# Kernel tuning notes

Measured on AMD Instinct MI355X. Metric: run time of the kernel, lower is better.

Reference implementation:

```python
import jax, jax.numpy as jnp
import numpy as np

REG_COEF = 25.0


def _reflect(points, planes):
    # points: [B,P,3], planes: [B,4] -> reflected points [B,P,3]
    normals = planes[:, 0:3] / jnp.linalg.norm(planes[:, 0:3], axis=1, keepdims=True)
    offsets = planes[:, 3]
    # signed distance of each point to the plane: [B,P]
    dist = jnp.einsum('bd,bpd->bp', normals, points) + offsets[:, None]
    return points - 2.0 * dist[..., None] * normals[:, None, :]


def _chamfer(x, y):
    # x,y: [B,P,3]; pytorch3d chamfer_distance default:
    # mean over points, mean over batch, sum of both directions (squared dists)
    x2 = jnp.sum(x * x, axis=-1)  # [B,P]
    y2 = jnp.sum(y * y, axis=-1)  # [B,P]
    # pairwise squared distances [B,P,P]
    d = x2[:, :, None] + y2[:, None, :] - 2.0 * jnp.einsum('bpd,bqd->bpq', x, y)
    d = jnp.maximum(d, 0.0)
    cham_x = jnp.mean(jnp.min(d, axis=2))  # x -> nearest in y
    cham_y = jnp.mean(jnp.min(d, axis=1))  # y -> nearest in x
    return cham_x + cham_y


def _reg_loss(planes):
    # planes: [B,H,4]
    normals = planes[:, :, :3]
    normals = normals / jnp.linalg.norm(normals, axis=2, keepdims=True)
    H = normals.shape[1]
    a = jnp.einsum('bhd,bgd->bhg', normals, normals) - jnp.eye(H, dtype=normals.dtype)
    # Frobenius norm per batch -> [B]
    return jnp.sqrt(jnp.sum(a * a, axis=(1, 2)))


def setup_inputs() -> dict:
    key = jax.random.key(0)
    k1, k2 = jax.random.split(key)
    B, H, P = 8, 3, 4096
    return {
        'predicted_planes': jax.random.normal(k1, (B, H, 4), dtype=jnp.float32),
        'sample_points': jax.random.normal(k2, (B, P, 3), dtype=jnp.float32),
        'voxel_grids': jnp.zeros((B, 32, 32, 32), dtype=jnp.float32),
        'cp_grids': jnp.zeros((B, 32, 32, 32), dtype=jnp.float32),
    }


def reference(predicted_planes, sample_points, voxel_grids, cp_grids):
    n_heads = predicted_planes.shape[1]
    reg = jnp.sum(_reg_loss(predicted_planes))
    refl = jnp.asarray(0.0, dtype=sample_points.dtype)
    for h in range(n_heads):  # small fixed head count (3)
        reflected = _reflect(sample_points, predicted_planes[:, h, :])
        refl = refl + _chamfer(sample_points, reflected)
    return refl + REG_COEF * reg
```

## Files before the change

kernel.cpp:

```cpp
#include <hip/hip_runtime.h>
#include <math.h>

#define NB 8
#define NH 3
#define NBH 24
#define NP 4096
#define BLK 256
#define RPB 128
#define ROWBLKS (NP / RPB)

typedef _Float16 half4 __attribute__((ext_vector_type(4)));
typedef float floatx16 __attribute__((ext_vector_type(16)));

#define MIN3(r, a, b) asm("v_min3_f32 %0, %0, %1, %2" : "+v"(r) : "v"(a), "v"(b))

#define MFMA8(d, a, bb, c) \
    asm("v_mfma_f32_32x32x8_f16 %0, %1, %2, %3" : "=&v"(d) : "v"(a), "v"(bb), "v"(c))

__global__ void reg_kernel(const float* __restrict__ planes, float* __restrict__ out) {
    const int l = threadIdx.x;
    float r = 0.0f;
    if (l < NB) {
        float n[NH][3];
        for (int hh = 0; hh < NH; ++hh) {
            const float* pl = planes + (l * NH + hh) * 4;
            float a0 = pl[0], a1 = pl[1], a2 = pl[2];
            float inv = 1.0f / sqrtf(a0 * a0 + a1 * a1 + a2 * a2);
            n[hh][0] = a0 * inv; n[hh][1] = a1 * inv; n[hh][2] = a2 * inv;
        }
        float fro = 0.0f;
        for (int i = 0; i < NH; ++i)
            for (int j = 0; j < NH; ++j) {
                float d = n[i][0] * n[j][0] + n[i][1] * n[j][1] + n[i][2] * n[j][2]
                          - (i == j ? 1.0f : 0.0f);
                fro += d * d;
            }
        r = 25.0f * sqrtf(fro);
    }
    for (int o = 32; o; o >>= 1) r += __shfl_down(r, o);
    if (l == 0) out[0] = r;
}

__global__ void __launch_bounds__(BLK, 3) chamfer_mfma(const float* __restrict__ pts,
                                                       const float* __restrict__ planes,
                                                       float* __restrict__ out) {
    __shared__ _Float16 qcols[NP * 4];
    __shared__ float rsqbuf[RPB];
    __shared__ float bsum[4];

    const int tid  = threadIdx.x;
    const int lane = tid & 63;
    const int wave = tid >> 6;
    const int bh   = blockIdx.y;
    const int b    = bh / NH;

    const float* pl = planes + bh * 4;
    float n0 = pl[0], n1 = pl[1], n2 = pl[2], off = pl[3];
    float inv = 1.0f / sqrtf(n0 * n0 + n1 * n1 + n2 * n2);
    n0 *= inv; n1 *= inv; n2 *= inv;

    const float* bp = pts + (size_t)b * NP * 3;
    const int h = lane >> 5;

    float total = 0.0f;

    for (int dir = 0; dir < 2; ++dir) {
        for (int i = tid; i < NP; i += BLK) {
            float y0 = bp[i * 3 + 0], y1 = bp[i * 3 + 1], y2 = bp[i * 3 + 2];
            if (!dir) { float t = 2.0f * (n0 * y0 + n1 * y1 + n2 * y2 + off); y0 -= t * n0; y1 -= t * n1; y2 -= t * n2; }
            float csq = y0 * y0 + y1 * y1 + y2 * y2;
            half4 v = { (_Float16)(-2.0f * y0), (_Float16)(-2.0f * y1),
                        (_Float16)(-2.0f * y2), (_Float16)csq };
            *(half4*)&qcols[i * 4] = v;
        }

        const int rlocal = wave * 32 + (lane & 31);
        const int row = blockIdx.x * RPB + rlocal;
        half4 afrag = {0, 0, 0, 0};
        {
            float a0 = bp[row * 3 + 0], a1 = bp[row * 3 + 1], a2 = bp[row * 3 + 2];
            if (dir) { float t = 2.0f * (n0 * a0 + n1 * a1 + n2 * a2 + off); a0 -= t * n0; a1 -= t * n1; a2 -= t * n2; }
            if (lane < 32) {
                rsqbuf[rlocal] = a0 * a0 + a1 * a1 + a2 * a2;
                afrag[0] = (_Float16)a0; afrag[1] = (_Float16)a1;
                afrag[2] = (_Float16)a2; afrag[3] = (_Float16)1.0f;
            }
        }
        __syncthreads();

        floatx16 crsq;
        #pragma unroll
        for (int j = 0; j < 16; ++j)
            crsq[j] = rsqbuf[wave * 32 + (j & 3) + 8 * (j >> 2) + 4 * h];

        float rm[16];
        #pragma unroll
        for (int j = 0; j < 16; ++j) rm[j] = 1e30f;

        const _Float16* bcol = &qcols[(lane & 31) * 4];

        half4 c0 = *(const half4*)(bcol);
        half4 c1 = *(const half4*)(bcol + 128);
        #pragma unroll 1
        for (int t = 0; t < 126; t += 2) {
            floatx16 d0, d1;
            MFMA8(d0, afrag, c0, crsq);
            MFMA8(d1, afrag, c1, crsq);
            c0 = *(const half4*)(bcol + (t + 2) * 128);
            c1 = *(const half4*)(bcol + (t + 3) * 128);
            #pragma unroll
            for (int j = 0; j < 16; ++j)
                MIN3(rm[j], d0[j], d1[j]);
        }
        {
            floatx16 d0, d1;
            MFMA8(d0, afrag, c0, crsq);
            MFMA8(d1, afrag, c1, crsq);
            #pragma unroll
            for (int j = 0; j < 16; ++j)
                MIN3(rm[j], d0[j], d1[j]);
        }

        #pragma unroll
        for (int j = 0; j < 16; ++j) {
            float v = rm[j];
            v = fminf(v, __shfl_xor(v, 1));
            v = fminf(v, __shfl_xor(v, 2));
            v = fminf(v, __shfl_xor(v, 4));
            v = fminf(v, __shfl_xor(v, 8));
            v = fminf(v, __shfl_xor(v, 16));
            rm[j] = v;
        }
        float s = 0.0f;
        #pragma unroll
        for (int j = 0; j < 16; ++j) s += fmaxf(rm[j], 0.0f);
        s += __shfl_xor(s, 32);
        total += s;

        __syncthreads();
    }

    if (lane == 0) bsum[wave] = total;
    __syncthreads();
    if (tid == 0)
        atomicAdd(out, (bsum[0] + bsum[1] + bsum[2] + bsum[3]) * (1.0f / (float)(NB * NP)));
}

extern "C" void kernel_launch(void* const* d_in, const int* in_sizes, int n_in,
                              void* d_out, int out_size, void* d_ws, size_t ws_size,
                              hipStream_t stream) {
    const float* planes = (const float*)d_in[0];
    const float* pts    = (const float*)d_in[1];
    float* out          = (float*)d_out;

    reg_kernel<<<1, 64, 0, stream>>>(planes, out);

    dim3 grid(ROWBLKS, NBH);
    chamfer_mfma<<<grid, BLK, 0, stream>>>(pts, planes, out);
}
```

Baseline: 94.31 us.

## Load 8-half column pairs and software-pipeline MFMA with min reduction

Each lane now reads 8 halves (two consecutive columns) per LDS load instead of 4, which halves the number of LDS reads. The loop is restructured into a two-stage software pipeline: the MFMAs for the next column pair are issued before the min3 reduction of the previous results, so matrix-core latency overlaps with VALU work. The column-to-lane mapping changes, but every column is still covered. The cost is more live accumulator registers (four floatx16), which may reduce occupancy.

```diff
diff --git a/kernel.cpp b/kernel.cpp
--- a/kernel.cpp
+++ b/kernel.cpp
@@ -10,12 +10,16 @@
 #define ROWBLKS (NP / RPB)
 
 typedef _Float16 half4 __attribute__((ext_vector_type(4)));
+typedef _Float16 half8 __attribute__((ext_vector_type(8)));
 typedef float floatx16 __attribute__((ext_vector_type(16)));
 
 #define MIN3(r, a, b) asm("v_min3_f32 %0, %0, %1, %2" : "+v"(r) : "v"(a), "v"(b))
 
 #define MFMA8(d, a, bb, c) \
     asm("v_mfma_f32_32x32x8_f16 %0, %1, %2, %3" : "=&v"(d) : "v"(a), "v"(bb), "v"(c))
+
+#define LO4(c8) __builtin_shufflevector(c8, c8, 0, 1, 2, 3)
+#define HI4(c8) __builtin_shufflevector(c8, c8, 4, 5, 6, 7)
 
 __global__ void reg_kernel(const float* __restrict__ planes, float* __restrict__ out) {
     const int l = threadIdx.x;
@@ -97,28 +101,35 @@
         #pragma unroll
         for (int j = 0; j < 16; ++j) rm[j] = 1e30f;
 
-        const _Float16* bcol = &qcols[(lane & 31) * 4];
+        const _Float16* bcol = &qcols[(lane & 31) * 8];
 
-        half4 c0 = *(const half4*)(bcol);
-        half4 c1 = *(const half4*)(bcol + 128);
+        half8 cc0 = *(const half8*)(bcol);
+        half8 cc1 = *(const half8*)(bcol + 256);
+        floatx16 dA0, dA1, dB0, dB1;
+        MFMA8(dA0, afrag, LO4(cc0), crsq);
+        MFMA8(dA1, afrag, HI4(cc0), crsq);
+
         #pragma unroll 1
-        for (int t = 0; t < 126; t += 2) {
-            floatx16 d0, d1;
-            MFMA8(d0, afrag, c0, crsq);
-            MFMA8(d1, afrag, c1, crsq);
-            c0 = *(const half4*)(bcol + (t + 2) * 128);
-            c1 = *(const half4*)(bcol + (t + 3) * 128);
+        for (int u = 2; u < 64; u += 2) {
+            half8 nc0 = *(const half8*)(bcol + u * 256);
+            MFMA8(dB0, afrag, LO4(cc1), crsq);
+            MFMA8(dB1, afrag, HI4(cc1), crsq);
             #pragma unroll
-            for (int j = 0; j < 16; ++j)
-                MIN3(rm[j], d0[j], d1[j]);
+            for (int j = 0; j < 16; ++j) MIN3(rm[j], dA0[j], dA1[j]);
+            half8 nc1 = *(const half8*)(bcol + (u + 1) * 256);
+            MFMA8(dA0, afrag, LO4(nc0), crsq);
+            MFMA8(dA1, afrag, HI4(nc0), crsq);
+            #pragma unroll
+            for (int j = 0; j < 16; ++j) MIN3(rm[j], dB0[j], dB1[j]);
+            cc1 = nc1;
         }
         {
-            floatx16 d0, d1;
-            MFMA8(d0, afrag, c0, crsq);
-            MFMA8(d1, afrag, c1, crsq);
+            MFMA8(dB0, afrag, LO4(cc1), crsq);
+            MFMA8(dB1, afrag, HI4(cc1), crsq);
             #pragma unroll
-            for (int j = 0; j < 16; ++j)
-                MIN3(rm[j], d0[j], d1[j]);
+            for (int j = 0; j < 16; ++j) MIN3(rm[j], dA0[j], dA1[j]);
+            #pragma unroll
+            for (int j = 0; j < 16; ++j) MIN3(rm[j], dB0[j], dB1[j]);
         }
 
         #pragma unroll
```

Result: no change. 93.23 us (-1.1%).
